# Optimization experiments

Hardware: AMD Instinct MI355X
Metric: run time of the kernel (lower is better)

## Reference

```python
import jax, jax.numpy as jnp
import numpy as np

EMBED_DIM = 1024
NUM_HEADS = 16
HEAD_DIM = EMBED_DIM // NUM_HEADS


def setup_inputs() -> dict:
    key = jax.random.key(0)
    ks = jax.random.split(key, 5)
    B, S, D = 2, 2048, EMBED_DIM
    bound_qkv = 1.0 / np.sqrt(D)
    bound_out = 1.0 / np.sqrt(D)
    return {
        "x": jax.random.normal(ks[0], (B, S, D), dtype=jnp.float32),
        "w_qkv": jax.random.uniform(ks[1], (3 * D, D), jnp.float32, -bound_qkv, bound_qkv),
        "b_qkv": jax.random.uniform(ks[2], (3 * D,), jnp.float32, -bound_qkv, bound_qkv),
        "w_out": jax.random.uniform(ks[3], (D, D), jnp.float32, -bound_out, bound_out),
        "b_out": jax.random.uniform(ks[4], (D,), jnp.float32, -bound_out, bound_out),
    }


def reference(x, w_qkv, b_qkv, w_out, b_out):
    B, S, D = x.shape
    H, Hd = NUM_HEADS, HEAD_DIM
    qkv = x @ w_qkv.T + b_qkv                      # [B,S,3D]
    q, k, v = jnp.split(qkv, 3, axis=-1)           # each [B,S,D]
    # [B,S,D] -> [B,H,S,Hd]
    q = q.reshape(B, S, H, Hd).transpose(0, 2, 1, 3)
    k = k.reshape(B, S, H, Hd).transpose(0, 2, 1, 3)
    v = v.reshape(B, S, H, Hd).transpose(0, 2, 1, 3)
    scores = jnp.einsum("bhqd,bhkd->bhqk", q, k) / np.sqrt(Hd).astype(np.float32)
    probs = jax.nn.softmax(scores, axis=-1)
    attn = jnp.einsum("bhqk,bhkd->bhqd", probs, v)  # [B,H,S,Hd]
    attn = attn.transpose(0, 2, 1, 3).reshape(B, S, D)
    return attn @ w_out.T + b_out
```

## Files before the change

### kernel.cpp

```cpp
#include <hip/hip_runtime.h>

typedef __bf16 bf16_t;
typedef bf16_t bf16x4 __attribute__((ext_vector_type(4)));
typedef bf16_t bf16x8 __attribute__((ext_vector_type(8)));
typedef float f32x4 __attribute__((ext_vector_type(4)));
typedef float f32x16 __attribute__((ext_vector_type(16)));
typedef unsigned short u16;

#define MFMA16(a, b, c) __builtin_amdgcn_mfma_f32_16x16x32_bf16((a), (b), (c), 0, 0, 0)
#define MFMA32(a, b, c) __builtin_amdgcn_mfma_f32_32x32x16_bf16((a), (b), (c), 0, 0, 0)

#define BATCH 2
#define SEQ   2048
#define DIM   1024
#define NH    16
#define HD    64
#define ROWS  (BATCH * SEQ)
#define QKVN  (3 * DIM)
#define GK    1024

__device__ __forceinline__ u16 f2bf(float f) {
    unsigned u = __float_as_uint(f);
    u += 0x7FFFu + ((u >> 16) & 1u);
    return (u16)(u >> 16);
}

__device__ __forceinline__ float exp2_fast(float x) {
    float r;
    asm("v_exp_f32 %0, %1" : "=v"(r) : "v"(x));
    return r;
}

#define PKBF(lo_, hi_) ({ unsigned r_; \
    asm("v_cvt_pk_bf16_f32 %0, %1, %2" : "=v"(r_) : "v"(lo_), "v"(hi_)); r_; })
#define PLSWAP(a_, b_) \
    asm volatile("v_permlane32_swap_b32 %0, %1" : "+v"(a_), "+v"(b_))

#define GLDS(src, dst) __builtin_amdgcn_global_load_lds( \
    (const __attribute__((address_space(1))) void*)(src), \
    (__attribute__((address_space(3))) void*)(dst), 16, 0, 0)

__global__ __launch_bounds__(256) void cvt_kernel(
    const float* __restrict__ x,  u16* __restrict__ xb,  int nx4,
    const float* __restrict__ w1, u16* __restrict__ w1b, int n14,
    const float* __restrict__ w2, u16* __restrict__ w2b, int n24)
{
    const int total = nx4 + n14 + n24;
    for (int i = blockIdx.x * 256 + threadIdx.x; i < total; i += gridDim.x * 256) {
        const float4* s; ushort4* d; int o;
        if (i < nx4)             { s = (const float4*)x;  d = (ushort4*)xb;  o = i; }
        else if (i < nx4 + n14)  { s = (const float4*)w1; d = (ushort4*)w1b; o = i - nx4; }
        else                     { s = (const float4*)w2; d = (ushort4*)w2b; o = i - nx4 - n14; }
        float4 v = s[o];
        ushort4 r;
        r.x = f2bf(v.x); r.y = f2bf(v.y); r.z = f2bf(v.z); r.w = f2bf(v.w);
        d[o] = r;
    }
}

__global__ __launch_bounds__(512, 1) void gemm_qkv256(
    const u16* __restrict__ A, const u16* __restrict__ Bt,
    const float* __restrict__ bias, u16* __restrict__ C)
{
    __shared__ u16 As[2][256 * 64];
    __shared__ u16 Bs[2][192 * 64];

    const int tid  = threadIdx.x;
    const int lane = tid & 63;
    const int wave = tid >> 6;
    const int r16  = lane & 15;
    const int grp  = lane >> 4;
    const int wm   = wave >> 2, wn = wave & 3;

    int v = (int)blockIdx.x;
    v = (v & 7) * 32 + (v >> 3);
    const int tm = v >> 4, tn = v & 15;
    const size_t brow = (size_t)tm * 256;
    const size_t bcol = (size_t)tn * 192;

    const int srow = tid >> 3;
    const int aoff = ((tid & 7) ^ (srow & 7)) * 8;
    const u16* pA = A  + (brow + srow) * (size_t)GK + aoff;
    const u16* pB = Bt + (bcol + srow) * (size_t)GK + aoff;

    f32x4 acc[8][3];
    const f32x4 fz = {0.f, 0.f, 0.f, 0.f};
    #pragma unroll
    for (int m = 0; m < 8; ++m)
        #pragma unroll
        for (int n = 0; n < 3; ++n) acc[m][n] = fz;

    const int sw = r16 & 7;
    #define LDA256(buf, mh, mm, ks) \
        (*(const bf16x8*)&(buf)[(wm*128 + (mh)*64 + (mm)*16 + r16)*64 + ((((ks)*4+grp)^sw)*8)])
    #define LDB256(buf, n, ks) \
        (*(const bf16x8*)&(buf)[(wn*48 + (n)*16 + r16)*64 + ((((ks)*4+grp)^sw)*8)])

    {
        u16* Ad = &As[0][(wave * 8) * 64];
        u16* Bd = &Bs[0][(wave * 8) * 64];
        GLDS(pA, Ad);                       GLDS(pA + 64 * GK,  Ad + 64 * 64);
        GLDS(pA + 128 * GK, Ad + 128 * 64); GLDS(pA + 192 * GK, Ad + 192 * 64);
        GLDS(pB, Bd);                       GLDS(pB + 64 * GK,  Bd + 64 * 64);
        GLDS(pB + 128 * GK, Bd + 128 * 64);
    }

    for (int kt = 0; kt < GK / 64; ++kt) {
        const int cur  = kt & 1;
        const bool last = (kt == GK / 64 - 1);
        const int nk = (kt + 1) * 64;
        const u16* Ab = &As[cur][0];
        const u16* Bb = &Bs[cur][0];
        u16* Ad = &As[cur ^ 1][(wave * 8) * 64];
        u16* Bd = &Bs[cur ^ 1][(wave * 8) * 64];
        bf16x8 a[4][2], b0[2][2], b1[2];

        if (!last) {
            GLDS(pA + nk, Ad); GLDS(pA + 64 * GK + nk, Ad + 64 * 64);
            asm volatile("s_waitcnt vmcnt(2)" ::: "memory");
        } else {
            asm volatile("s_waitcnt vmcnt(0)" ::: "memory");
        }
        __builtin_amdgcn_s_barrier();
        #pragma unroll
        for (int mm = 0; mm < 4; ++mm) {
            a[mm][0] = LDA256(Ab, 0, mm, 0); a[mm][1] = LDA256(Ab, 0, mm, 1);
        }
        #pragma unroll
        for (int nn = 0; nn < 2; ++nn) {
            b0[nn][0] = LDB256(Bb, nn, 0); b0[nn][1] = LDB256(Bb, nn, 1);
        }
        __builtin_amdgcn_s_setprio(1);
        #pragma unroll
        for (int mm = 0; mm < 4; ++mm)
            #pragma unroll
            for (int nn = 0; nn < 2; ++nn) {
                acc[mm][nn] = MFMA16(a[mm][0], b0[nn][0], acc[mm][nn]);
                acc[mm][nn] = MFMA16(a[mm][1], b0[nn][1], acc[mm][nn]);
            }
        __builtin_amdgcn_s_setprio(0);
        __builtin_amdgcn_s_barrier();

        if (!last) { GLDS(pA + 128 * GK + nk, Ad + 128 * 64);
                     GLDS(pA + 192 * GK + nk, Ad + 192 * 64); }
        b1[0] = LDB256(Bb, 2, 0); b1[1] = LDB256(Bb, 2, 1);
        __builtin_amdgcn_s_setprio(1);
        #pragma unroll
        for (int mm = 0; mm < 4; ++mm) {
            acc[mm][2] = MFMA16(a[mm][0], b1[0], acc[mm][2]);
            acc[mm][2] = MFMA16(a[mm][1], b1[1], acc[mm][2]);
        }
        __builtin_amdgcn_s_setprio(0);
        __builtin_amdgcn_s_barrier();

        if (!last) { GLDS(pB + nk, Bd); GLDS(pB + 64 * GK + nk, Bd + 64 * 64); }
        #pragma unroll
        for (int mm = 0; mm < 4; ++mm) {
            a[mm][0] = LDA256(Ab, 1, mm, 0); a[mm][1] = LDA256(Ab, 1, mm, 1);
        }
        __builtin_amdgcn_s_setprio(1);
        #pragma unroll
        for (int mm = 0; mm < 4; ++mm) {
            acc[mm + 4][2] = MFMA16(a[mm][0], b1[0], acc[mm + 4][2]);
            acc[mm + 4][2] = MFMA16(a[mm][1], b1[1], acc[mm + 4][2]);
        }
        __builtin_amdgcn_s_setprio(0);
        __builtin_amdgcn_s_barrier();

        if (!last) { GLDS(pB + 128 * GK + nk, Bd + 128 * 64); }
        __builtin_amdgcn_s_setprio(1);
        #pragma unroll
        for (int mm = 0; mm < 4; ++mm)
            #pragma unroll
            for (int nn = 0; nn < 2; ++nn) {
                acc[mm + 4][nn] = MFMA16(a[mm][0], b0[nn][0], acc[mm + 4][nn]);
                acc[mm + 4][nn] = MFMA16(a[mm][1], b0[nn][1], acc[mm + 4][nn]);
            }
        __builtin_amdgcn_s_setprio(0);
        __builtin_amdgcn_s_barrier();
    }

    #pragma unroll
    for (int n = 0; n < 3; ++n) {
        const size_t col = bcol + wn * 48 + n * 16 + r16;
        const float bv = bias[col];
        #pragma unroll
        for (int m = 0; m < 8; ++m) {
            const size_t row0 = brow + wm * 128 + m * 16 + grp * 4;
            if ((int)col >= 2 * DIM) {
                const int c2 = (int)col - 2 * DIM;
                const int d = c2 & 63, h = c2 >> 6;
                const int bb = (int)(row0 >> 11), s0 = (int)(row0 & 2047);
                ushort4 pv;
                pv.x = f2bf(acc[m][n][0] + bv);
                pv.y = f2bf(acc[m][n][1] + bv);
                pv.z = f2bf(acc[m][n][2] + bv);
                pv.w = f2bf(acc[m][n][3] + bv);
                u16* dst = C + ((size_t)bb * 2048 + d * 32 + (s0 >> 6)) * (size_t)QKVN
                             + 2 * DIM + h * 64 + (s0 & 63);
                *(ushort4*)dst = pv;
            } else {
                #pragma unroll
                for (int i = 0; i < 4; ++i)
                    C[(row0 + i) * (size_t)QKVN + col] = f2bf(acc[m][n][i] + bv);
            }
        }
    }
    #undef LDA256
    #undef LDB256
}

__global__ __launch_bounds__(256) void gemm_bt(
    const u16* __restrict__ A, const u16* __restrict__ Bt,
    const float* __restrict__ bias, float* __restrict__ Cv,
    int M, int N, int K)
{
    __shared__ u16 As[128 * 64];
    __shared__ u16 Bs[64 * 64];

    const int tid  = threadIdx.x;
    const int lane = tid & 63;
    const int wave = tid >> 6;
    const int r16  = lane & 15;
    const int grp  = lane >> 4;

    const int nt  = N >> 6;
    const int nwg = (M >> 7) * nt;
    int v = blockIdx.x;
    if ((nwg & 7) == 0) { const int cpx = nwg >> 3; v = (v & 7) * cpx + (v >> 3); }
    const int tm = v / nt, tn = v - tm * nt;
    const size_t brow = (size_t)tm << 7;
    const size_t bcol = (size_t)tn << 6;

    const int wr = wave >> 1, wc = wave & 1;

    f32x4 acc[4][2];
    const f32x4 fz = {0.f, 0.f, 0.f, 0.f};
    #pragma unroll
    for (int m = 0; m < 4; ++m)
        #pragma unroll
        for (int n = 0; n < 2; ++n) acc[m][n] = fz;

    for (int kt = 0; kt < K; kt += 64) {
        #pragma unroll
        for (int it = 0; it < 4; ++it) {
            const int c = it * 256 + tid;
            const u16* ga = A + (brow + (c >> 3)) * (size_t)K + kt + (c & 7) * 8;
            GLDS(ga, &As[(it * 256 + wave * 64) * 8]);
        }
        #pragma unroll
        for (int it = 0; it < 2; ++it) {
            const int c = it * 256 + tid;
            const u16* gb = Bt + (bcol + (c >> 3)) * (size_t)K + kt + (c & 7) * 8;
            GLDS(gb, &Bs[(it * 256 + wave * 64) * 8]);
        }
        __syncthreads();
        #pragma unroll
        for (int ks = 0; ks < 2; ++ks) {
            bf16x8 af[4], bfr[2];
            #pragma unroll
            for (int m = 0; m < 4; ++m)
                af[m] = *(const bf16x8*)&As[(wr * 64 + m * 16 + r16) * 64 + ks * 32 + grp * 8];
            #pragma unroll
            for (int n = 0; n < 2; ++n)
                bfr[n] = *(const bf16x8*)&Bs[(wc * 32 + n * 16 + r16) * 64 + ks * 32 + grp * 8];
            #pragma unroll
            for (int m = 0; m < 4; ++m)
                #pragma unroll
                for (int n = 0; n < 2; ++n)
                    acc[m][n] = MFMA16(af[m], bfr[n], acc[m][n]);
        }
        __syncthreads();
    }

    #pragma unroll
    for (int n = 0; n < 2; ++n) {
        const size_t col = bcol + wc * 32 + n * 16 + r16;
        const float bv = bias[col];
        #pragma unroll
        for (int m = 0; m < 4; ++m) {
            const size_t row0 = brow + wr * 64 + m * 16 + grp * 4;
            #pragma unroll
            for (int i = 0; i < 4; ++i)
                Cv[(row0 + i) * (size_t)N + col] = acc[m][n][i] + bv;
        }
    }
}

__global__ __launch_bounds__(512, 4) void attn_kernel(
    const u16* __restrict__ qkv, u16* __restrict__ attb)
{
    __shared__ u16 smem[18432];

    const int tid  = threadIdx.x;
    const int lane = tid & 63;
    const int wave = tid >> 6;
    const int half = wave >> 2;
    const int w4   = wave & 3;
    const int l31  = lane & 31;
    const int hi   = lane >> 5;
    const int k7   = l31 & 7;

    u16* khalf = smem + half * 8192;
    u16* vhalf = smem + half * 8192 + 4096;

    int v = (int)blockIdx.x;
    v = (v & 7) * 64 + (v >> 3);
    const int bh = v >> 4, qblk = v & 15;
    const int b  = bh >> 4, h = bh & 15;
    const int bS = b * SEQ;
    const int q0w = qblk * 128 + w4 * 32;

    bf16x8 qf[4];
    {
        const u16* qp = qkv + (size_t)(bS + q0w + l31) * QKVN + h * HD + hi * 8;
        #pragma unroll
        for (int m = 0; m < 4; ++m) qf[m] = *(const bf16x8*)(qp + m * 16);
    }

    const f32x16 fz16 = {0,0,0,0,0,0,0,0,0,0,0,0,0,0,0,0};
    f32x16 o0 = fz16, o1 = fz16;
    float lsum = 0.f;

    const int r0 = w4 * 16 + (lane >> 3);
    const int r1 = r0 + 8;
    const u16* kbase = qkv + (size_t)bS * QKVN + DIM + h * HD;
    const char* kp0 = (const char*)(kbase + (size_t)(r0 + half * 1024) * QKVN)
                      + (((lane & 7) * 16) ^ ((r0 & 7) << 4));
    const char* kp1 = (const char*)(kbase + (size_t)(r1 + half * 1024) * QKVN)
                      + (((lane & 7) * 16) ^ ((r1 & 7) << 4));
    const u16* vtb = qkv + (size_t)bS * QKVN + 2 * DIM + h * HD;
    const char* vp0 = (const char*)(vtb + (size_t)(r0 * 32 + half * 16) * QKVN)
                      + (((lane & 7) * 16) ^ ((r0 & 7) << 4));
    const char* vp1 = (const char*)(vtb + (size_t)(r1 * 32 + half * 16) * QKVN)
                      + (((lane & 7) * 16) ^ ((r1 & 7) << 4));

    u16* kd = khalf + (w4 * 16) * 64;
    u16* vd = vhalf + (w4 * 16) * 64;

    auto stage = [&]() {
        GLDS(kp0, kd);
        GLDS(kp1, kd + 8 * 64);
        GLDS(vp0, vd);
        GLDS(vp1, vd + 8 * 64);
        kp0 += 64 * QKVN * 2; kp1 += 64 * QKVN * 2;
        vp0 += QKVN * 2;      vp1 += QKVN * 2;
    };

    const float C1 = 0.125f * 1.44269504f;
    const float C2 = -8.0f * 1.44269504f;

    auto compute_tile = [&](const u16* kb_, const u16* vb_) {
        const char* kc = (const char*)kb_;
        const char* vc = (const char*)vb_;
        bf16x8 paf[4];

        #pragma unroll
        for (int kt = 0; kt < 2; ++kt) {
            bf16x8 kf[4];
            #pragma unroll
            for (int m = 0; m < 4; ++m)
                kf[m] = *(const bf16x8*)(kc + (kt * 32 + l31) * 128
                                            + (((m * 2 + hi) ^ k7) * 16));
            f32x16 s = fz16;
            __builtin_amdgcn_s_setprio(1);
            #pragma unroll
            for (int m = 0; m < 4; ++m) s = MFMA32(kf[m], qf[m], s);
            __builtin_amdgcn_s_setprio(0);

            float p[16];
            #pragma unroll
            for (int r = 0; r < 16; ++r) {
                p[r] = exp2_fast(fmaf(s[r], C1, C2));
                lsum += p[r];
            }
            unsigned A = PKBF(p[0], p[1]),  Bw = PKBF(p[2], p[3]);
            unsigned C = PKBF(p[4], p[5]),  D  = PKBF(p[6], p[7]);
            unsigned E = PKBF(p[8], p[9]),  F  = PKBF(p[10], p[11]);
            unsigned G = PKBF(p[12], p[13]), H = PKBF(p[14], p[15]);
            PLSWAP(A, C); PLSWAP(Bw, D); PLSWAP(E, G); PLSWAP(F, H);
            union { unsigned u[4]; bf16x8 v8; } w0 = {{A, Bw, C, D}},
                                                w1 = {{E, F, G, H}};
            paf[kt * 2]     = w0.v8;
            paf[kt * 2 + 1] = w1.v8;
        }

        __builtin_amdgcn_s_setprio(1);
        #pragma unroll
        for (int m2 = 0; m2 < 4; ++m2) {
            const int cs = ((m2 * 2 + hi) ^ k7) * 16;
            const bf16x8 vf0 = *(const bf16x8*)(vc + l31 * 128 + cs);
            const bf16x8 vf1 = *(const bf16x8*)(vc + (32 + l31) * 128 + cs);
            o0 = MFMA32(paf[m2], vf0, o0);
            o1 = MFMA32(paf[m2], vf1, o1);
        }
        __builtin_amdgcn_s_setprio(0);
    };

    for (int t = 0; t < 16; ++t) {
        stage();
        asm volatile("s_waitcnt vmcnt(0)" ::: "memory");
        __builtin_amdgcn_s_barrier();
        compute_tile(khalf, vhalf);
        __builtin_amdgcn_s_barrier();
    }

    float* obuf = (float*)smem;
    const int cidx = (w4 * 64 + lane) * 36;
    if (half == 1) {
        #pragma unroll
        for (int r = 0; r < 16; ++r) {
            obuf[cidx + r]      = o0[r];
            obuf[cidx + 16 + r] = o1[r];
        }
        obuf[cidx + 32] = lsum;
    }
    __syncthreads();
    if (half == 0) {
        #pragma unroll
        for (int r = 0; r < 16; ++r) {
            o0[r] += obuf[cidx + r];
            o1[r] += obuf[cidx + 16 + r];
        }
        lsum += obuf[cidx + 32];

        const float ltot = lsum + __shfl_xor(lsum, 32, 64);
        const float rinv = 1.0f / ltot;

        u16* ob = attb + (size_t)(bS + q0w) * DIM + h * HD + l31;
        #pragma unroll
        for (int r = 0; r < 16; ++r) {
            const int q = (r & 3) + 8 * (r >> 2) + 4 * hi;
            const float iv = __shfl(rinv, q, 64);
            u16* pr = ob + (size_t)q * DIM;
            pr[0]  = f2bf(o0[r] * iv);
            pr[32] = f2bf(o1[r] * iv);
        }
    }
}

extern "C" void kernel_launch(void* const* d_in, const int* in_sizes, int n_in,
                              void* d_out, int out_size, void* d_ws, size_t ws_size,
                              hipStream_t stream)
{
    const float* x     = (const float*)d_in[0];
    const float* w_qkv = (const float*)d_in[1];
    const float* b_qkv = (const float*)d_in[2];
    const float* w_out = (const float*)d_in[3];
    const float* b_out = (const float*)d_in[4];
    float* out = (float*)d_out;

    u16* ws   = (u16*)d_ws;
    u16* XB   = ws;
    u16* WQB  = ws + 4194304;
    u16* WOB  = ws + 7340032;
    u16* QKVB = ws + 8388608;
    u16* ATTB = ws + 20971520;

    cvt_kernel<<<2048, 256, 0, stream>>>(x, XB, (ROWS * DIM) / 4,
                                         w_qkv, WQB, (QKVN * DIM) / 4,
                                         w_out, WOB, (DIM * DIM) / 4);

    gemm_qkv256<<<(ROWS / 256) * (QKVN / 192), 512, 0, stream>>>(
        XB, WQB, b_qkv, QKVB);

    attn_kernel<<<BATCH * NH * (SEQ / 128), 512, 0, stream>>>(QKVB, ATTB);

    gemm_bt<<<(ROWS / 128) * (DIM / 64), 256, 0, stream>>>(
        ATTB, WOB, b_out, out, ROWS, DIM, GK);
}
```

Before: 119.9 us.

## Double-buffer output GEMM loads and split attention KV range four ways

The output-projection GEMM gains a double-buffered LDS ring, so the next K tile's global-to-LDS loads are issued before computing the current one, with partial vmcnt waits and raised MFMA priority. The attention kernel moves to 1024 threads per block, splitting the key/value sequence into four quarter ranges (one per wave group) instead of two halves. The four partial accumulators are then reduced through LDS in three serialized rounds. This adds LDS use and barriers, and larger blocks may reduce occupancy, in exchange for more parallelism per query tile and overlap of loads with compute.

```diff
diff --git a/kernel.cpp b/kernel.cpp
--- a/kernel.cpp
+++ b/kernel.cpp
@@ -215,8 +215,8 @@
     const float* __restrict__ bias, float* __restrict__ Cv,
     int M, int N, int K)
 {
-    __shared__ u16 As[128 * 64];
-    __shared__ u16 Bs[64 * 64];
+    __shared__ u16 As[2][128 * 64];
+    __shared__ u16 Bs[2][64 * 64];
 
     const int tid  = threadIdx.x;
     const int lane = tid & 63;
@@ -241,36 +241,52 @@
         #pragma unroll
         for (int n = 0; n < 2; ++n) acc[m][n] = fz;
 
-    for (int kt = 0; kt < K; kt += 64) {
+    auto stage = [&](int buf, int kt) {
         #pragma unroll
         for (int it = 0; it < 4; ++it) {
             const int c = it * 256 + tid;
             const u16* ga = A + (brow + (c >> 3)) * (size_t)K + kt + (c & 7) * 8;
-            GLDS(ga, &As[(it * 256 + wave * 64) * 8]);
+            GLDS(ga, &As[buf][(it * 256 + wave * 64) * 8]);
         }
         #pragma unroll
         for (int it = 0; it < 2; ++it) {
             const int c = it * 256 + tid;
             const u16* gb = Bt + (bcol + (c >> 3)) * (size_t)K + kt + (c & 7) * 8;
-            GLDS(gb, &Bs[(it * 256 + wave * 64) * 8]);
-        }
-        __syncthreads();
+            GLDS(gb, &Bs[buf][(it * 256 + wave * 64) * 8]);
+        }
+    };
+
+    stage(0, 0);
+    const int nkt = K >> 6;
+    for (int kt = 0; kt < nkt; ++kt) {
+        const int buf = kt & 1;
+        if (kt < nkt - 1) {
+            stage(buf ^ 1, (kt + 1) << 6);
+            asm volatile("s_waitcnt vmcnt(6)" ::: "memory");
+        } else {
+            asm volatile("s_waitcnt vmcnt(0)" ::: "memory");
+        }
+        __builtin_amdgcn_s_barrier();
+        const u16* Ab = &As[buf][0];
+        const u16* Bb = &Bs[buf][0];
         #pragma unroll
         for (int ks = 0; ks < 2; ++ks) {
             bf16x8 af[4], bfr[2];
             #pragma unroll
             for (int m = 0; m < 4; ++m)
-                af[m] = *(const bf16x8*)&As[(wr * 64 + m * 16 + r16) * 64 + ks * 32 + grp * 8];
+                af[m] = *(const bf16x8*)&Ab[(wr * 64 + m * 16 + r16) * 64 + ks * 32 + grp * 8];
             #pragma unroll
             for (int n = 0; n < 2; ++n)
-                bfr[n] = *(const bf16x8*)&Bs[(wc * 32 + n * 16 + r16) * 64 + ks * 32 + grp * 8];
+                bfr[n] = *(const bf16x8*)&Bb[(wc * 32 + n * 16 + r16) * 64 + ks * 32 + grp * 8];
+            __builtin_amdgcn_s_setprio(1);
             #pragma unroll
             for (int m = 0; m < 4; ++m)
                 #pragma unroll
                 for (int n = 0; n < 2; ++n)
                     acc[m][n] = MFMA16(af[m], bfr[n], acc[m][n]);
-        }
-        __syncthreads();
+            __builtin_amdgcn_s_setprio(0);
+        }
+        __builtin_amdgcn_s_barrier();
     }
 
     #pragma unroll
@@ -287,29 +303,29 @@
     }
 }
 
-__global__ __launch_bounds__(512, 4) void attn_kernel(
+__global__ __launch_bounds__(1024, 4) void attn_kernel(
     const u16* __restrict__ qkv, u16* __restrict__ attb)
 {
-    __shared__ u16 smem[18432];
+    __shared__ u16 smem[32768];
 
     const int tid  = threadIdx.x;
     const int lane = tid & 63;
     const int wave = tid >> 6;
-    const int half = wave >> 2;
-    const int w4   = wave & 3;
+    const int qb   = wave >> 2;
+    const int qq   = wave & 3;
     const int l31  = lane & 31;
     const int hi   = lane >> 5;
     const int k7   = l31 & 7;
 
-    u16* khalf = smem + half * 8192;
-    u16* vhalf = smem + half * 8192 + 4096;
+    u16* kq = smem + qq * 8192;
+    u16* vq = kq + 4096;
 
     int v = (int)blockIdx.x;
     v = (v & 7) * 64 + (v >> 3);
     const int bh = v >> 4, qblk = v & 15;
     const int b  = bh >> 4, h = bh & 15;
     const int bS = b * SEQ;
-    const int q0w = qblk * 128 + w4 * 32;
+    const int q0w = qblk * 128 + qb * 32;
 
     bf16x8 qf[4];
     {
@@ -322,21 +338,21 @@
     f32x16 o0 = fz16, o1 = fz16;
     float lsum = 0.f;
 
-    const int r0 = w4 * 16 + (lane >> 3);
+    const int r0 = qb * 16 + (lane >> 3);
     const int r1 = r0 + 8;
     const u16* kbase = qkv + (size_t)bS * QKVN + DIM + h * HD;
-    const char* kp0 = (const char*)(kbase + (size_t)(r0 + half * 1024) * QKVN)
+    const char* kp0 = (const char*)(kbase + (size_t)(r0 + qq * 512) * QKVN)
                       + (((lane & 7) * 16) ^ ((r0 & 7) << 4));
-    const char* kp1 = (const char*)(kbase + (size_t)(r1 + half * 1024) * QKVN)
+    const char* kp1 = (const char*)(kbase + (size_t)(r1 + qq * 512) * QKVN)
                       + (((lane & 7) * 16) ^ ((r1 & 7) << 4));
     const u16* vtb = qkv + (size_t)bS * QKVN + 2 * DIM + h * HD;
-    const char* vp0 = (const char*)(vtb + (size_t)(r0 * 32 + half * 16) * QKVN)
+    const char* vp0 = (const char*)(vtb + (size_t)(r0 * 32 + qq * 8) * QKVN)
                       + (((lane & 7) * 16) ^ ((r0 & 7) << 4));
-    const char* vp1 = (const char*)(vtb + (size_t)(r1 * 32 + half * 16) * QKVN)
+    const char* vp1 = (const char*)(vtb + (size_t)(r1 * 32 + qq * 8) * QKVN)
                       + (((lane & 7) * 16) ^ ((r1 & 7) << 4));
 
-    u16* kd = khalf + (w4 * 16) * 64;
-    u16* vd = vhalf + (w4 * 16) * 64;
+    u16* kd = kq + (qb * 16) * 64;
+    u16* vd = vq + (qb * 16) * 64;
 
     auto stage = [&]() {
         GLDS(kp0, kd);
@@ -350,9 +366,9 @@
     const float C1 = 0.125f * 1.44269504f;
     const float C2 = -8.0f * 1.44269504f;
 
-    auto compute_tile = [&](const u16* kb_, const u16* vb_) {
-        const char* kc = (const char*)kb_;
-        const char* vc = (const char*)vb_;
+    auto compute_tile = [&]() {
+        const char* kc = (const char*)kq;
+        const char* vc = (const char*)vq;
         bf16x8 paf[4];
 
         #pragma unroll
@@ -397,33 +413,39 @@
         __builtin_amdgcn_s_setprio(0);
     };
 
-    for (int t = 0; t < 16; ++t) {
+    for (int t = 0; t < 8; ++t) {
         stage();
         asm volatile("s_waitcnt vmcnt(0)" ::: "memory");
         __builtin_amdgcn_s_barrier();
-        compute_tile(khalf, vhalf);
+        compute_tile();
         __builtin_amdgcn_s_barrier();
     }
 
     float* obuf = (float*)smem;
-    const int cidx = (w4 * 64 + lane) * 36;
-    if (half == 1) {
-        #pragma unroll
-        for (int r = 0; r < 16; ++r) {
-            obuf[cidx + r]      = o0[r];
-            obuf[cidx + 16 + r] = o1[r];
-        }
-        obuf[cidx + 32] = lsum;
-    }
-    __syncthreads();
-    if (half == 0) {
-        #pragma unroll
-        for (int r = 0; r < 16; ++r) {
-            o0[r] += obuf[cidx + r];
-            o1[r] += obuf[cidx + 16 + r];
-        }
-        lsum += obuf[cidx + 32];
-
+    const int cidx = (qb * 64 + lane) * 34;
+    #pragma unroll
+    for (int rr = 1; rr < 4; ++rr) {
+        if (qq == rr) {
+            #pragma unroll
+            for (int r = 0; r < 16; ++r) {
+                obuf[cidx + r]      = o0[r];
+                obuf[cidx + 16 + r] = o1[r];
+            }
+            obuf[cidx + 32] = lsum;
+        }
+        __syncthreads();
+        if (qq == 0) {
+            #pragma unroll
+            for (int r = 0; r < 16; ++r) {
+                o0[r] += obuf[cidx + r];
+                o1[r] += obuf[cidx + 16 + r];
+            }
+            lsum += obuf[cidx + 32];
+        }
+        __syncthreads();
+    }
+
+    if (qq == 0) {
         const float ltot = lsum + __shfl_xor(lsum, 32, 64);
         const float rinv = 1.0f / ltot;
 
@@ -464,7 +486,7 @@
     gemm_qkv256<<<(ROWS / 256) * (QKVN / 192), 512, 0, stream>>>(
         XB, WQB, b_qkv, QKVB);
 
-    attn_kernel<<<BATCH * NH * (SEQ / 128), 512, 0, stream>>>(QKVB, ATTB);
+    attn_kernel<<<BATCH * NH * (SEQ / 128), 1024, 0, stream>>>(QKVB, ATTB);
 
     gemm_bt<<<(ROWS / 128) * (DIM / 64), 256, 0, stream>>>(
         ATTB, WOB, b_out, out, ROWS, DIM, GK);
```

New measurement: 131.7 us. 1.1x slower.
